# Optimization experiments

Measured on AMD Instinct MI355X. Metric: run time of the kernel, lower is better.

The kernel has to match this reference:

```python
import jax, jax.numpy as jnp
import numpy as np

N = 100000
E = 1600000
F_IN = 256
H1, C1 = 8, 8          # conv1: 8 heads x 8 channels -> 64
H2, C2 = 1, 32         # conv2: 1 head x num_classes
SLOPE = 0.2


def gat_conv(x, src, dst, n, W, a_src, a_dst, b, heads, out):
    # x: [n, f_in]; W: [f_in, heads*out]; a_src/a_dst: [heads, out]; b: [heads*out]
    h = (x @ W).reshape(n, heads, out)                       # [n, H, C]
    s = jnp.sum(h * a_src, axis=-1)                          # [n, H]
    d = jnp.sum(h * a_dst, axis=-1)                          # [n, H]
    e = jax.nn.leaky_relu(s[src] + d[dst], SLOPE)            # [e, H]
    m = jax.ops.segment_max(e, dst, num_segments=n)          # stable segment softmax
    ex = jnp.exp(e - m[dst])
    z = jax.ops.segment_sum(ex, dst, num_segments=n)
    alpha = ex / (z[dst] + 1e-16)                            # [e, H]
    msg = alpha[:, :, None] * h[src]                         # [e, H, C]
    agg = jax.ops.segment_sum(msg, dst, num_segments=n)      # [n, H, C]
    return agg.reshape(n, heads * out) + b


def setup_inputs() -> dict:
    key = jax.random.key(0)
    ks = jax.random.split(key, 10)
    x = jax.random.normal(ks[0], (N, F_IN), dtype=jnp.float32)
    edge_index = jax.random.randint(ks[1], (2, E), 0, N, dtype=jnp.int32)
    sc = 0.05
    W1 = jax.random.normal(ks[2], (F_IN, H1 * C1), dtype=jnp.float32) * sc
    att_src1 = jax.random.normal(ks[3], (H1, C1), dtype=jnp.float32) * sc
    att_dst1 = jax.random.normal(ks[4], (H1, C1), dtype=jnp.float32) * sc
    b1 = jnp.zeros((H1 * C1,), dtype=jnp.float32)
    W2 = jax.random.normal(ks[5], (H1 * C1, H2 * C2), dtype=jnp.float32) * sc
    att_src2 = jax.random.normal(ks[6], (H2, C2), dtype=jnp.float32) * sc
    att_dst2 = jax.random.normal(ks[7], (H2, C2), dtype=jnp.float32) * sc
    b2 = jnp.zeros((H2 * C2,), dtype=jnp.float32)
    return {"x": x, "edge_index": edge_index, "W1": W1, "att_src1": att_src1,
            "att_dst1": att_dst1, "b1": b1, "W2": W2, "att_src2": att_src2,
            "att_dst2": att_dst2, "b2": b2}


def reference(x, edge_index, W1, att_src1, att_dst1, b1, W2, att_src2, att_dst2, b2):
    # add self loops (PyG GATConv default)
    loops = jnp.arange(N, dtype=edge_index.dtype)
    src = jnp.concatenate([edge_index[0], loops])
    dst = jnp.concatenate([edge_index[1], loops])
    # dropout layers are identity in eval mode
    h = gat_conv(x, src, dst, N, W1, att_src1, att_dst1, b1, H1, C1)
    h = jax.nn.elu(h)
    h = gat_conv(h, src, dst, N, W2, att_src2, att_dst2, b2, H2, C2)
    return jax.nn.log_softmax(h, axis=1)
```

## Files before the change

### kernel.cpp

```cpp
#include <hip/hip_runtime.h>
#include <hip/hip_bf16.h>

#define N_NODES 100000
#define N_EDGES 1600000
#define N_TOT   (N_EDGES + N_NODES)
#define F_IN    256
#define F1      64
#define H1      8
#define C1      8
#define F2      32
#define SLOPE   0.2f
#define CHUNK   2048
#define NCH     ((N_NODES + CHUNK - 1) / CHUNK)

#define NB_G    ((N_NODES + 255) / 256)

#define EB      4096
#define NB1     ((N_EDGES + EB - 1) / EB)
#define BW      256
#define NBKT    ((N_NODES + BW - 1) / BW)

typedef unsigned int  uint;
typedef unsigned short ushort;
typedef __attribute__((ext_vector_type(8))) short bf16x8;
typedef __attribute__((ext_vector_type(4))) float f32x4;
typedef __attribute__((ext_vector_type(2))) float f32x2;

__device__ inline ushort f2bf(float f) {
    uint u = __float_as_uint(f);
    uint r = u + 0x7fffu + ((u >> 16) & 1u);
    return (ushort)(r >> 16);
}
__device__ inline float bflo(uint u) { return __uint_as_float(u << 16); }
__device__ inline float bfhi(uint u) { return __uint_as_float(u & 0xffff0000u); }
__device__ inline uint pk2bf(float a, float b) {
    __hip_bfloat162 h = __float22bfloat162_rn(make_float2(a, b));
    union { __hip_bfloat162 h; uint u; } cv; cv.h = h;
    return cv.u;
}

__device__ inline void bucket_bases(const int* __restrict__ colsum,
                                    int* sc, int* sb, int tid) {
    const int i0 = 2 * tid, i1 = 2 * tid + 1;
    const int a0 = (i0 < NBKT) ? colsum[i0] : 0;
    const int a1 = (i1 < NBKT) ? colsum[i1] : 0;
    sc[tid] = a0 + a1;
    __syncthreads();
    for (int off = 1; off < 256; off <<= 1) {
        int t = (tid >= off) ? sc[tid - off] : 0;
        __syncthreads();
        sc[tid] += t;
        __syncthreads();
    }
    const int excl = sc[tid] - (a0 + a1);
    if (i0 < NBKT)  sb[i0] = excl;
    if (i1 <= NBKT) sb[i1] = excl + a0;
    __syncthreads();
}

__global__ __launch_bounds__(256) void k_gemm1_p1(
        const float* __restrict__ x, const float* __restrict__ W1,
        const float* __restrict__ as1, const float* __restrict__ ad1,
        const int* __restrict__ ei,
        ushort* __restrict__ h1b, float* __restrict__ s1, float* __restrict__ d1,
        int* __restrict__ bcnt) {
    __shared__ union {
        ushort B[F_IN * F1];
        ushort S[4][64][66];
        int    H[NBKT];
    } sm;
    const int tid = threadIdx.x;

    if (blockIdx.x >= NB_G) {
        const int blk = blockIdx.x - NB_G;
        for (int j = tid; j < NBKT; j += 256) sm.H[j] = 0;
        __syncthreads();
        const int e0 = blk * EB;
        const int lim = (e0 + EB < N_EDGES) ? e0 + EB : N_EDGES;
        for (int i = e0 + tid; i < lim; i += 256)
            atomicAdd(&sm.H[ei[N_EDGES + i] >> 8], 1);
        __syncthreads();
        for (int j = tid; j < NBKT; j += 256)
            bcnt[j * NB1 + blk] = sm.H[j];
        return;
    }

    for (int i = 0; i < 64; ++i) {
        const int e = i * 256 + tid;
        const int k = e >> 6, n = e & 63;
        sm.B[((k >> 3) * 64 + n) * 8 + (k & 7)] = f2bf(W1[e]);
    }
    __syncthreads();

    const int wave = tid >> 6, lane = tid & 63;
    const int q = lane >> 4, ln = lane & 15;
    const int rowbase = blockIdx.x * 256 + wave * 64;

    f32x4 acc[4][4];
#pragma unroll
    for (int mt = 0; mt < 4; ++mt)
#pragma unroll
        for (int nt = 0; nt < 4; ++nt) acc[mt][nt] = (f32x4){0.f, 0.f, 0.f, 0.f};

    int rows[4];
#pragma unroll
    for (int mt = 0; mt < 4; ++mt) {
        const int r = rowbase + mt * 16 + ln;
        rows[mt] = r < N_NODES ? r : N_NODES - 1;
    }

    for (int t = 0; t < 8; ++t) {
        bf16x8 bfr[4];
#pragma unroll
        for (int nt = 0; nt < 4; ++nt)
            bfr[nt] = *(const bf16x8*)&sm.B[((t * 4 + q) * 64 + nt * 16 + ln) * 8];
#pragma unroll
        for (int mt = 0; mt < 4; ++mt) {
            const float4* ap = (const float4*)(x + (size_t)rows[mt] * F_IN + t * 32 + q * 8);
            const float4 a0 = ap[0], a1 = ap[1];
            uint4 au = make_uint4(pk2bf(a0.x, a0.y), pk2bf(a0.z, a0.w),
                                  pk2bf(a1.x, a1.y), pk2bf(a1.z, a1.w));
            bf16x8 af = *(bf16x8*)&au;
#pragma unroll
            for (int nt = 0; nt < 4; ++nt)
                acc[mt][nt] = __builtin_amdgcn_mfma_f32_16x16x32_bf16(
                                  af, bfr[nt], acc[mt][nt], 0, 0, 0);
        }
    }
    __syncthreads();

#pragma unroll
    for (int mt = 0; mt < 4; ++mt)
#pragma unroll
        for (int nt = 0; nt < 4; ++nt)
#pragma unroll
            for (int r = 0; r < 4; ++r)
                sm.S[wave][mt * 16 + q * 4 + r][nt * 16 + ln] = f2bf(acc[mt][nt][r]);
    __syncthreads();

    const int node = rowbase + lane;
    if (node >= N_NODES) return;
    const uint* srow = (const uint*)&sm.S[wave][lane][0];
    float sacc[H1], dacc[H1];
#pragma unroll
    for (int h = 0; h < H1; ++h) { sacc[h] = 0.f; dacc[h] = 0.f; }
    uint4* hout = (uint4*)(h1b + (size_t)node * F1);
#pragma unroll
    for (int p4 = 0; p4 < 8; ++p4) {
        const uint u0 = srow[p4 * 4 + 0], u1 = srow[p4 * 4 + 1];
        const uint u2 = srow[p4 * 4 + 2], u3 = srow[p4 * 4 + 3];
        hout[p4] = make_uint4(u0, u1, u2, u3);
        const float c[8] = {bflo(u0), bfhi(u0), bflo(u1), bfhi(u1),
                            bflo(u2), bfhi(u2), bflo(u3), bfhi(u3)};
#pragma unroll
        for (int j = 0; j < 8; ++j) {
            sacc[p4] += c[j] * as1[p4 * 8 + j];
            dacc[p4] += c[j] * ad1[p4 * 8 + j];
        }
    }
    float4* s4 = (float4*)(s1 + (size_t)node * H1);
    float4* d4 = (float4*)(d1 + (size_t)node * H1);
    s4[0] = make_float4(sacc[0], sacc[1], sacc[2], sacc[3]);
    s4[1] = make_float4(sacc[4], sacc[5], sacc[6], sacc[7]);
    d4[0] = make_float4(dacc[0], dacc[1], dacc[2], dacc[3]);
    d4[1] = make_float4(dacc[4], dacc[5], dacc[6], dacc[7]);
}

__global__ __launch_bounds__(64) void k_p2(
        int* __restrict__ bcnt, int* __restrict__ colsum) {
    const int col = blockIdx.x, lane = threadIdx.x;
    int carry = 0;
    for (int c0 = 0; c0 < NB1; c0 += 64) {
        const int idx = c0 + lane;
        const int v = (idx < NB1) ? bcnt[col * NB1 + idx] : 0;
        int s = v;
#pragma unroll
        for (int off = 1; off < 64; off <<= 1) {
            int u = __shfl_up(s, off);
            if (lane >= off) s += u;
        }
        if (idx < NB1) bcnt[col * NB1 + idx] = carry + s - v;
        carry += __shfl(s, 63);
    }
    if (lane == 0) colsum[col] = carry;
}

__global__ __launch_bounds__(256) void k_p3(
        const int* __restrict__ ei, const int* __restrict__ bcnt,
        const int* __restrict__ colsum, int2* __restrict__ tmp) {
    __shared__ int sc[256];
    __shared__ int cur[NBKT + 1];
    const int tid = threadIdx.x, blk = blockIdx.x;
    bucket_bases(colsum, sc, cur, tid);
    for (int b = tid; b < NBKT; b += 256) cur[b] += bcnt[b * NB1 + blk];
    __syncthreads();
    const int e0 = blk * EB;
    const int lim = (e0 + EB < N_EDGES) ? e0 + EB : N_EDGES;
    for (int i = e0 + tid; i < lim; i += 256) {
        const int s = ei[i], d = ei[N_EDGES + i];
        const int pos = atomicAdd(&cur[d >> 8], 1);
        tmp[pos] = make_int2(s, d);
    }
}

__global__ __launch_bounds__(256) void k_p4(
        const int2* __restrict__ tmp, const int* __restrict__ colsum,
        int* __restrict__ cnt) {
    __shared__ int sc[256];
    __shared__ int sb[NBKT + 1];
    __shared__ int h[BW];
    const int tid = threadIdx.x, b = blockIdx.x;
    bucket_bases(colsum, sc, sb, tid);
    h[tid] = 0;
    __syncthreads();
    const int lo = sb[b], hi = sb[b + 1];
    for (int i = lo + tid; i < hi; i += 256)
        atomicAdd(&h[tmp[i].y & (BW - 1)], 1);
    __syncthreads();
    const int n = b * BW + tid;
    if (n < N_NODES) cnt[n] = h[tid];
}

__global__ __launch_bounds__(256) void k_scan_a(
        const int* __restrict__ cnt, int* __restrict__ row_ptr,
        int* __restrict__ bsum) {
    __shared__ int sdata[256];
    const int tid = threadIdx.x;
    const int base = blockIdx.x * CHUNK + tid * 8;
    int v[8];
    int tot = 0;
#pragma unroll
    for (int j = 0; j < 8; ++j) {
        v[j] = (base + j < N_NODES) ? cnt[base + j] + 1 : 0;
        tot += v[j];
    }
    sdata[tid] = tot;
    __syncthreads();
    for (int off = 1; off < 256; off <<= 1) {
        int t = (tid >= off) ? sdata[tid - off] : 0;
        __syncthreads();
        sdata[tid] += t;
        __syncthreads();
    }
    int run = sdata[tid] - tot;
#pragma unroll
    for (int j = 0; j < 8; ++j) {
        if (base + j < N_NODES) row_ptr[base + j] = run;
        run += v[j];
    }
    if (tid == 255) bsum[blockIdx.x] = sdata[255];
}

__global__ __launch_bounds__(256) void k_scan_c2(
        int* __restrict__ row_ptr, const int* __restrict__ bsum,
        int* __restrict__ srcs) {
    __shared__ int pb[64];
    const int t = threadIdx.x;
    if (t < 64) {
        int v = (t < NCH) ? bsum[t] : 0;
        const int orig = v;
        for (int off = 1; off < 64; off <<= 1) {
            int u = __shfl_up(v, off);
            if (t >= off) v += u;
        }
        pb[t] = v - orig;
    }
    __syncthreads();
    const int i = blockIdx.x * 256 + t;
    if (i < N_NODES) {
        const int rp = row_ptr[i] + pb[i / CHUNK];
        row_ptr[i] = rp;
        srcs[rp] = i;
    } else if (i == N_NODES) row_ptr[N_NODES] = N_TOT;
}

__global__ __launch_bounds__(256) void k_p6(
        const int2* __restrict__ tmp, const int* __restrict__ colsum,
        const int* __restrict__ row_ptr, int* __restrict__ srcs) {
    __shared__ int sc[256];
    __shared__ int sb[NBKT + 1];
    __shared__ int rp[BW];
    __shared__ int cur[BW];
    const int tid = threadIdx.x, b = blockIdx.x;
    bucket_bases(colsum, sc, sb, tid);
    const int n = b * BW + tid;
    rp[tid] = (n < N_NODES) ? row_ptr[n] : 0;
    cur[tid] = 0;
    __syncthreads();
    const int lo = sb[b], hi = sb[b + 1];
    for (int i = lo + tid; i < hi; i += 256) {
        const int2 e = tmp[i];
        const int loc = e.y & (BW - 1);
        const int r = atomicAdd(&cur[loc], 1);
        srcs[rp[loc] + 1 + r] = e.x;
    }
}

__global__ __launch_bounds__(256) void k_agg1(
        const int* __restrict__ row_ptr, const int* __restrict__ srcs,
        const ushort* __restrict__ h1b, const float* __restrict__ s1,
        const float* __restrict__ d1, const float* __restrict__ b1,
        const float* __restrict__ W2, const float* __restrict__ as2,
        const float* __restrict__ ad2,
        ushort* __restrict__ h2b, float* __restrict__ s2,
        float* __restrict__ d2) {
    __shared__ float sx[4][64];
    const int wid = (blockIdx.x * 256 + threadIdx.x) >> 6;
    if (wid >= N_NODES) return;
    const int w = threadIdx.x >> 6;
    const int lane = threadIdx.x & 63;
    const int q = lane >> 3;
    const int c = lane & 7;
    const float dh = d1[(size_t)wid * H1 + c];
    const int beg = row_ptr[wid], end = row_ptr[wid + 1];
    const uint4* hv = (const uint4*)h1b;
    f32x2 A0 = {0.f, 0.f}, A1 = {0.f, 0.f}, A2 = {0.f, 0.f}, A3 = {0.f, 0.f};
    float z = 0.f;
    int i = beg + q;
    for (; i + 8 < end; i += 16) {
        const int sA = srcs[i], sB = srcs[i + 8];
        float eA = s1[(size_t)sA * H1 + c] + dh;
        float eB = s1[(size_t)sB * H1 + c] + dh;
        eA = fmaxf(eA, SLOPE * eA);
        eB = fmaxf(eB, SLOPE * eB);
        const float xA = __expf(eA), xB = __expf(eB);
        const uint4 UA = hv[(size_t)sA * 8 + c];
        const uint4 UB = hv[(size_t)sB * 8 + c];
        z += xA + xB;
        const f32x2 xa = {xA, xA}, xb = {xB, xB};
        A0 += xa * (f32x2){bflo(UA.x), bfhi(UA.x)};
        A1 += xa * (f32x2){bflo(UA.y), bfhi(UA.y)};
        A2 += xa * (f32x2){bflo(UA.z), bfhi(UA.z)};
        A3 += xa * (f32x2){bflo(UA.w), bfhi(UA.w)};
        A0 += xb * (f32x2){bflo(UB.x), bfhi(UB.x)};
        A1 += xb * (f32x2){bflo(UB.y), bfhi(UB.y)};
        A2 += xb * (f32x2){bflo(UB.z), bfhi(UB.z)};
        A3 += xb * (f32x2){bflo(UB.w), bfhi(UB.w)};
    }
    for (; i < end; i += 8) {
        const int sA = srcs[i];
        float eA = s1[(size_t)sA * H1 + c] + dh;
        eA = fmaxf(eA, SLOPE * eA);
        const float xA = __expf(eA);
        const uint4 UA = hv[(size_t)sA * 8 + c];
        z += xA;
        const f32x2 xa = {xA, xA};
        A0 += xa * (f32x2){bflo(UA.x), bfhi(UA.x)};
        A1 += xa * (f32x2){bflo(UA.y), bfhi(UA.y)};
        A2 += xa * (f32x2){bflo(UA.z), bfhi(UA.z)};
        A3 += xa * (f32x2){bflo(UA.w), bfhi(UA.w)};
    }
    f32x2 r0, r1;
    {
        const bool hi = lane & 8;
        f32x2 snd0 = hi ? A0 : A2, snd1 = hi ? A1 : A3;
        const f32x2 kp0 = hi ? A2 : A0, kp1 = hi ? A3 : A1;
        snd0.x = __shfl_xor(snd0.x, 8); snd0.y = __shfl_xor(snd0.y, 8);
        snd1.x = __shfl_xor(snd1.x, 8); snd1.y = __shfl_xor(snd1.y, 8);
        r0 = kp0 + snd0; r1 = kp1 + snd1;
    }
    {
        const bool hi = lane & 16;
        f32x2 snd = hi ? r0 : r1;
        const f32x2 kp = hi ? r1 : r0;
        snd.x = __shfl_xor(snd.x, 16); snd.y = __shfl_xor(snd.y, 16);
        r0 = kp + snd;
    }
    float sv;
    {
        const bool hi = lane & 32;
        float snd = hi ? r0.x : r0.y;
        const float kp = hi ? r0.y : r0.x;
        snd = __shfl_xor(snd, 32);
        sv = kp + snd;
    }
    z += __shfl_xor(z, 8); z += __shfl_xor(z, 16); z += __shfl_xor(z, 32);

    const int j = (((lane >> 3) & 1) << 2) | (((lane >> 4) & 1) << 1)
                | ((lane >> 5) & 1);
    const int xi = c * 8 + j;
    const float zi = 1.f / (z + 1e-16f);
    float xv = sv * zi + b1[xi];
    xv = xv > 0.f ? xv : __expf(xv) - 1.f;
    sx[w][xi] = xv;
    __builtin_amdgcn_wave_barrier();

    const int kh = lane >> 5;
    const int oc = lane & 31;
    const float4* sxv = (const float4*)&sx[w][kh * 32];
    const float* wp0 = W2 + (size_t)(kh * 32) * F2 + oc;
    float acc = 0.f;
#pragma unroll
    for (int k4 = 0; k4 < 8; ++k4) {
        const float4 xv4 = sxv[k4];
        const float* wp = wp0 + (size_t)k4 * 4 * F2;
        acc += xv4.x * wp[0]      + xv4.y * wp[F2]
             + xv4.z * wp[2 * F2] + xv4.w * wp[3 * F2];
    }
    acc += __shfl_xor(acc, 32);

    float sA2 = acc * as2[oc], dA2 = acc * ad2[oc];
#pragma unroll
    for (int off = 1; off <= 16; off <<= 1) {
        sA2 += __shfl_xor(sA2, off);
        dA2 += __shfl_xor(dA2, off);
    }
    const float accp = __shfl_xor(acc, 1);
    if (lane < 32 && !(lane & 1))
        *(uint*)&h2b[(size_t)wid * F2 + oc] = pk2bf(acc, accp);
    if (lane == 0) { s2[wid] = sA2; d2[wid] = dA2; }
}

__global__ __launch_bounds__(256) void k_agg2(
        const int* __restrict__ row_ptr, const int* __restrict__ srcs,
        const ushort* __restrict__ h2b, const float* __restrict__ s2,
        const float* __restrict__ d2, const float* __restrict__ b2,
        float* __restrict__ out) {
    const int wid = (blockIdx.x * 256 + threadIdx.x) >> 6;
    if (wid >= N_NODES) return;
    const int lane = threadIdx.x & 63;
    const int q = lane >> 2;
    const int c = lane & 3;
    const float dn = d2[wid];
    const int beg = row_ptr[wid], end = row_ptr[wid + 1];
    const uint4* hv = (const uint4*)h2b;
    f32x2 A0 = {0.f, 0.f}, A1 = {0.f, 0.f}, A2 = {0.f, 0.f}, A3 = {0.f, 0.f};
    float z = 0.f;
    int i = beg + q;
    for (; i + 16 < end; i += 32) {
        const int sA = srcs[i], sB = srcs[i + 16];
        float eA = s2[sA] + dn;
        float eB = s2[sB] + dn;
        eA = fmaxf(eA, SLOPE * eA);
        eB = fmaxf(eB, SLOPE * eB);
        const float xA = __expf(eA), xB = __expf(eB);
        const uint4 UA = hv[(size_t)sA * 4 + c];
        const uint4 UB = hv[(size_t)sB * 4 + c];
        z += xA + xB;
        const f32x2 xa = {xA, xA}, xb = {xB, xB};
        A0 += xa * (f32x2){bflo(UA.x), bfhi(UA.x)};
        A1 += xa * (f32x2){bflo(UA.y), bfhi(UA.y)};
        A2 += xa * (f32x2){bflo(UA.z), bfhi(UA.z)};
        A3 += xa * (f32x2){bflo(UA.w), bfhi(UA.w)};
        A0 += xb * (f32x2){bflo(UB.x), bfhi(UB.x)};
        A1 += xb * (f32x2){bflo(UB.y), bfhi(UB.y)};
        A2 += xb * (f32x2){bflo(UB.z), bfhi(UB.z)};
        A3 += xb * (f32x2){bflo(UB.w), bfhi(UB.w)};
    }
    for (; i < end; i += 16) {
        const int sA = srcs[i];
        float eA = s2[sA] + dn;
        eA = fmaxf(eA, SLOPE * eA);
        const float xA = __expf(eA);
        const uint4 UA = hv[(size_t)sA * 4 + c];
        z += xA;
        const f32x2 xa = {xA, xA};
        A0 += xa * (f32x2){bflo(UA.x), bfhi(UA.x)};
        A1 += xa * (f32x2){bflo(UA.y), bfhi(UA.y)};
        A2 += xa * (f32x2){bflo(UA.z), bfhi(UA.z)};
        A3 += xa * (f32x2){bflo(UA.w), bfhi(UA.w)};
    }
    f32x2 r0, r1;
    {
        const bool hi = lane & 4;
        f32x2 snd0 = hi ? A0 : A2, snd1 = hi ? A1 : A3;
        const f32x2 kp0 = hi ? A2 : A0, kp1 = hi ? A3 : A1;
        snd0.x = __shfl_xor(snd0.x, 4); snd0.y = __shfl_xor(snd0.y, 4);
        snd1.x = __shfl_xor(snd1.x, 4); snd1.y = __shfl_xor(snd1.y, 4);
        r0 = kp0 + snd0; r1 = kp1 + snd1;
    }
    {
        const bool hi = lane & 8;
        f32x2 snd = hi ? r0 : r1;
        const f32x2 kp = hi ? r1 : r0;
        snd.x = __shfl_xor(snd.x, 8); snd.y = __shfl_xor(snd.y, 8);
        r0 = kp + snd;
    }
    float sv;
    {
        const bool hi = lane & 16;
        float snd = hi ? r0.x : r0.y;
        const float kp = hi ? r0.y : r0.x;
        snd = __shfl_xor(snd, 16);
        sv = kp + snd;
    }
    sv += __shfl_xor(sv, 32);
    z += __shfl_xor(z, 4); z += __shfl_xor(z, 8);
    z += __shfl_xor(z, 16); z += __shfl_xor(z, 32);

    const int j = (((lane >> 2) & 1) << 2) | (((lane >> 3) & 1) << 1)
                | ((lane >> 4) & 1);
    const int elem = c * 8 + j;
    const float zi = 1.f / (z + 1e-16f);
    const float v = sv * zi + b2[elem];
    float m = v;
#pragma unroll
    for (int off = 1; off <= 16; off <<= 1) m = fmaxf(m, __shfl_xor(m, off));
    float ssum = __expf(v - m);
#pragma unroll
    for (int off = 1; off <= 16; off <<= 1) ssum += __shfl_xor(ssum, off);
    const float lse = m + __logf(ssum);
    if (lane < 32) out[(size_t)wid * F2 + elem] = v - lse;
}

extern "C" void kernel_launch(void* const* d_in, const int* in_sizes, int n_in,
                              void* d_out, int out_size, void* d_ws, size_t ws_size,
                              hipStream_t stream) {
    const float* x   = (const float*)d_in[0];
    const int*   ei  = (const int*)d_in[1];
    const float* W1  = (const float*)d_in[2];
    const float* as1 = (const float*)d_in[3];
    const float* ad1 = (const float*)d_in[4];
    const float* b1  = (const float*)d_in[5];
    const float* W2  = (const float*)d_in[6];
    const float* as2 = (const float*)d_in[7];
    const float* ad2 = (const float*)d_in[8];
    const float* b2  = (const float*)d_in[9];
    float* out = (float*)d_out;

    ushort* h1b = (ushort*)d_ws;
    ushort* h2b = h1b + (size_t)N_NODES * F1;
    float*  s1  = (float*)(h2b + (size_t)N_NODES * F2);
    float*  d1  = s1 + (size_t)N_NODES * H1;
    float*  s2  = d1 + (size_t)N_NODES * H1;
    float*  d2  = s2 + N_NODES;
    int2*   tmp = (int2*)(d2 + N_NODES);
    int* cnt     = (int*)(tmp + N_EDGES);
    int* row_ptr = cnt + N_NODES;
    int* bsum    = row_ptr + N_NODES + 1;
    int* colsum  = bsum + 64;
    int* bcnt    = colsum + NBKT;
    int* srcs    = bcnt + (size_t)NBKT * NB1;

    const int nb_w = (N_NODES * 64 + 255) / 256;

    k_gemm1_p1<<<NB_G + NB1, 256, 0, stream>>>(x, W1, as1, ad1, ei,
                                               h1b, s1, d1, bcnt);
    k_p2<<<NBKT, 64, 0, stream>>>(bcnt, colsum);
    k_p3<<<NB1, 256, 0, stream>>>(ei, bcnt, colsum, tmp);
    k_p4<<<NBKT, 256, 0, stream>>>(tmp, colsum, cnt);
    k_scan_a<<<NCH, 256, 0, stream>>>(cnt, row_ptr, bsum);
    k_scan_c2<<<(N_NODES + 256) / 256, 256, 0, stream>>>(row_ptr, bsum, srcs);
    k_p6<<<NBKT, 256, 0, stream>>>(tmp, colsum, row_ptr, srcs);
    k_agg1<<<nb_w, 256, 0, stream>>>(row_ptr, srcs, h1b, s1, d1, b1,
                                     W2, as2, ad2, h2b, s2, d2);
    k_agg2<<<nb_w, 256, 0, stream>>>(row_ptr, srcs, h2b, s2, d2, b2, out);
}
```

Measured before the change: 351.3 us.

## Fuse CSR build kernels, pack edge temp, and interleave s1 with h1 rows

Folds the per-bucket count, the two global scan kernels and the scatter into a single per-bucket kernel. Row offsets come from bucket bases plus a local scan, which removes three launches and a global cnt/row_ptr round trip. The temporary edge array is packed into one 32-bit word per edge (8-bit local dst, 24-bit src), halving that traffic. The layer-1 source logits s1 are stored in the same 160-byte row as the bf16 h1 features, so each gathered neighbour in aggregation touches one row instead of two separate arrays. The packing relies on node ids fitting in 24 bits and bucket width 256.

```diff
diff --git a/kernel.cpp b/kernel.cpp
--- a/kernel.cpp
+++ b/kernel.cpp
@@ -10,8 +10,6 @@
 #define C1      8
 #define F2      32
 #define SLOPE   0.2f
-#define CHUNK   2048
-#define NCH     ((N_NODES + CHUNK - 1) / CHUNK)
 
 #define NB_G    ((N_NODES + 255) / 256)
 
@@ -62,7 +60,7 @@
         const float* __restrict__ x, const float* __restrict__ W1,
         const float* __restrict__ as1, const float* __restrict__ ad1,
         const int* __restrict__ ei,
-        ushort* __restrict__ h1b, float* __restrict__ s1, float* __restrict__ d1,
+        uint* __restrict__ sh1, float* __restrict__ d1,
         int* __restrict__ bcnt) {
     __shared__ union {
         ushort B[F_IN * F1];
@@ -144,12 +142,12 @@
     float sacc[H1], dacc[H1];
 #pragma unroll
     for (int h = 0; h < H1; ++h) { sacc[h] = 0.f; dacc[h] = 0.f; }
-    uint4* hout = (uint4*)(h1b + (size_t)node * F1);
+    uint* rowp = sh1 + (size_t)node * 40;
 #pragma unroll
     for (int p4 = 0; p4 < 8; ++p4) {
         const uint u0 = srow[p4 * 4 + 0], u1 = srow[p4 * 4 + 1];
         const uint u2 = srow[p4 * 4 + 2], u3 = srow[p4 * 4 + 3];
-        hout[p4] = make_uint4(u0, u1, u2, u3);
+        ((uint4*)rowp)[2 + p4] = make_uint4(u0, u1, u2, u3);
         const float c[8] = {bflo(u0), bfhi(u0), bflo(u1), bfhi(u1),
                             bflo(u2), bfhi(u2), bflo(u3), bfhi(u3)};
 #pragma unroll
@@ -158,10 +156,9 @@
             dacc[p4] += c[j] * ad1[p4 * 8 + j];
         }
     }
-    float4* s4 = (float4*)(s1 + (size_t)node * H1);
+    ((float4*)rowp)[0] = make_float4(sacc[0], sacc[1], sacc[2], sacc[3]);
+    ((float4*)rowp)[1] = make_float4(sacc[4], sacc[5], sacc[6], sacc[7]);
     float4* d4 = (float4*)(d1 + (size_t)node * H1);
-    s4[0] = make_float4(sacc[0], sacc[1], sacc[2], sacc[3]);
-    s4[1] = make_float4(sacc[4], sacc[5], sacc[6], sacc[7]);
     d4[0] = make_float4(dacc[0], dacc[1], dacc[2], dacc[3]);
     d4[1] = make_float4(dacc[4], dacc[5], dacc[6], dacc[7]);
 }
@@ -187,7 +184,7 @@
 
 __global__ __launch_bounds__(256) void k_p3(
         const int* __restrict__ ei, const int* __restrict__ bcnt,
-        const int* __restrict__ colsum, int2* __restrict__ tmp) {
+        const int* __restrict__ colsum, uint* __restrict__ tmp) {
     __shared__ int sc[256];
     __shared__ int cur[NBKT + 1];
     const int tid = threadIdx.x, blk = blockIdx.x;
@@ -199,107 +196,54 @@
     for (int i = e0 + tid; i < lim; i += 256) {
         const int s = ei[i], d = ei[N_EDGES + i];
         const int pos = atomicAdd(&cur[d >> 8], 1);
-        tmp[pos] = make_int2(s, d);
-    }
-}
-
-__global__ __launch_bounds__(256) void k_p4(
-        const int2* __restrict__ tmp, const int* __restrict__ colsum,
-        int* __restrict__ cnt) {
+        tmp[pos] = ((uint)(d & 255) << 24) | (uint)s;
+    }
+}
+
+__global__ __launch_bounds__(256) void k_final(
+        const uint* __restrict__ tmp, const int* __restrict__ colsum,
+        int* __restrict__ row_ptr, int* __restrict__ srcs) {
     __shared__ int sc[256];
     __shared__ int sb[NBKT + 1];
-    __shared__ int h[BW];
-    const int tid = threadIdx.x, b = blockIdx.x;
-    bucket_bases(colsum, sc, sb, tid);
-    h[tid] = 0;
-    __syncthreads();
-    const int lo = sb[b], hi = sb[b + 1];
-    for (int i = lo + tid; i < hi; i += 256)
-        atomicAdd(&h[tmp[i].y & (BW - 1)], 1);
-    __syncthreads();
-    const int n = b * BW + tid;
-    if (n < N_NODES) cnt[n] = h[tid];
-}
-
-__global__ __launch_bounds__(256) void k_scan_a(
-        const int* __restrict__ cnt, int* __restrict__ row_ptr,
-        int* __restrict__ bsum) {
-    __shared__ int sdata[256];
-    const int tid = threadIdx.x;
-    const int base = blockIdx.x * CHUNK + tid * 8;
-    int v[8];
-    int tot = 0;
-#pragma unroll
-    for (int j = 0; j < 8; ++j) {
-        v[j] = (base + j < N_NODES) ? cnt[base + j] + 1 : 0;
-        tot += v[j];
-    }
-    sdata[tid] = tot;
-    __syncthreads();
-    for (int off = 1; off < 256; off <<= 1) {
-        int t = (tid >= off) ? sdata[tid - off] : 0;
-        __syncthreads();
-        sdata[tid] += t;
-        __syncthreads();
-    }
-    int run = sdata[tid] - tot;
-#pragma unroll
-    for (int j = 0; j < 8; ++j) {
-        if (base + j < N_NODES) row_ptr[base + j] = run;
-        run += v[j];
-    }
-    if (tid == 255) bsum[blockIdx.x] = sdata[255];
-}
-
-__global__ __launch_bounds__(256) void k_scan_c2(
-        int* __restrict__ row_ptr, const int* __restrict__ bsum,
-        int* __restrict__ srcs) {
-    __shared__ int pb[64];
-    const int t = threadIdx.x;
-    if (t < 64) {
-        int v = (t < NCH) ? bsum[t] : 0;
-        const int orig = v;
-        for (int off = 1; off < 64; off <<= 1) {
-            int u = __shfl_up(v, off);
-            if (t >= off) v += u;
-        }
-        pb[t] = v - orig;
-    }
-    __syncthreads();
-    const int i = blockIdx.x * 256 + t;
-    if (i < N_NODES) {
-        const int rp = row_ptr[i] + pb[i / CHUNK];
-        row_ptr[i] = rp;
-        srcs[rp] = i;
-    } else if (i == N_NODES) row_ptr[N_NODES] = N_TOT;
-}
-
-__global__ __launch_bounds__(256) void k_p6(
-        const int2* __restrict__ tmp, const int* __restrict__ colsum,
-        const int* __restrict__ row_ptr, int* __restrict__ srcs) {
-    __shared__ int sc[256];
-    __shared__ int sb[NBKT + 1];
-    __shared__ int rp[BW];
     __shared__ int cur[BW];
     const int tid = threadIdx.x, b = blockIdx.x;
     bucket_bases(colsum, sc, sb, tid);
+    cur[tid] = 0;
+    __syncthreads();
+    const int lo = sb[b], hi = sb[b + 1];
+    for (int i = lo + tid; i < hi; i += 256)
+        atomicAdd(&cur[tmp[i] >> 24], 1);
+    __syncthreads();
     const int n = b * BW + tid;
-    rp[tid] = (n < N_NODES) ? row_ptr[n] : 0;
-    cur[tid] = 0;
-    __syncthreads();
-    const int lo = sb[b], hi = sb[b + 1];
+    const int myc = cur[tid];
+    const int v = (n < N_NODES) ? myc + 1 : 0;
+    sc[tid] = v;
+    __syncthreads();
+    for (int off = 1; off < 256; off <<= 1) {
+        int t = (tid >= off) ? sc[tid - off] : 0;
+        __syncthreads();
+        sc[tid] += t;
+        __syncthreads();
+    }
+    const int rp = sb[b] + b * BW + (sc[tid] - v);
+    if (n < N_NODES) {
+        row_ptr[n] = rp;
+        srcs[rp] = n;
+    }
+    if (b == NBKT - 1 && tid == 255) row_ptr[N_NODES] = N_TOT;
+    cur[tid] = rp + 1;
+    __syncthreads();
     for (int i = lo + tid; i < hi; i += 256) {
-        const int2 e = tmp[i];
-        const int loc = e.y & (BW - 1);
-        const int r = atomicAdd(&cur[loc], 1);
-        srcs[rp[loc] + 1 + r] = e.x;
+        const uint u = tmp[i];
+        const int pos = atomicAdd(&cur[u >> 24], 1);
+        srcs[pos] = (int)(u & 0xFFFFFFu);
     }
 }
 
 __global__ __launch_bounds__(256) void k_agg1(
         const int* __restrict__ row_ptr, const int* __restrict__ srcs,
-        const ushort* __restrict__ h1b, const float* __restrict__ s1,
-        const float* __restrict__ d1, const float* __restrict__ b1,
+        const uint* __restrict__ sh1, const float* __restrict__ d1,
+        const float* __restrict__ b1,
         const float* __restrict__ W2, const float* __restrict__ as2,
         const float* __restrict__ ad2,
         ushort* __restrict__ h2b, float* __restrict__ s2,
@@ -311,21 +255,25 @@
     const int lane = threadIdx.x & 63;
     const int q = lane >> 3;
     const int c = lane & 7;
+    const int so = 4 * c;
+    const int ho = 32 + 16 * c;
     const float dh = d1[(size_t)wid * H1 + c];
     const int beg = row_ptr[wid], end = row_ptr[wid + 1];
-    const uint4* hv = (const uint4*)h1b;
+    const char* base = (const char*)sh1;
     f32x2 A0 = {0.f, 0.f}, A1 = {0.f, 0.f}, A2 = {0.f, 0.f}, A3 = {0.f, 0.f};
     float z = 0.f;
     int i = beg + q;
     for (; i + 8 < end; i += 16) {
         const int sA = srcs[i], sB = srcs[i + 8];
-        float eA = s1[(size_t)sA * H1 + c] + dh;
-        float eB = s1[(size_t)sB * H1 + c] + dh;
+        const char* rA = base + (size_t)sA * 160;
+        const char* rB = base + (size_t)sB * 160;
+        float eA = *(const float*)(rA + so) + dh;
+        float eB = *(const float*)(rB + so) + dh;
         eA = fmaxf(eA, SLOPE * eA);
         eB = fmaxf(eB, SLOPE * eB);
         const float xA = __expf(eA), xB = __expf(eB);
-        const uint4 UA = hv[(size_t)sA * 8 + c];
-        const uint4 UB = hv[(size_t)sB * 8 + c];
+        const uint4 UA = *(const uint4*)(rA + ho);
+        const uint4 UB = *(const uint4*)(rB + ho);
         z += xA + xB;
         const f32x2 xa = {xA, xA}, xb = {xB, xB};
         A0 += xa * (f32x2){bflo(UA.x), bfhi(UA.x)};
@@ -339,10 +287,11 @@
     }
     for (; i < end; i += 8) {
         const int sA = srcs[i];
-        float eA = s1[(size_t)sA * H1 + c] + dh;
+        const char* rA = base + (size_t)sA * 160;
+        float eA = *(const float*)(rA + so) + dh;
         eA = fmaxf(eA, SLOPE * eA);
         const float xA = __expf(eA);
-        const uint4 UA = hv[(size_t)sA * 8 + c];
+        const uint4 UA = *(const uint4*)(rA + ho);
         z += xA;
         const f32x2 xa = {xA, xA};
         A0 += xa * (f32x2){bflo(UA.x), bfhi(UA.x)};
@@ -518,31 +467,25 @@
     const float* b2  = (const float*)d_in[9];
     float* out = (float*)d_out;
 
-    ushort* h1b = (ushort*)d_ws;
-    ushort* h2b = h1b + (size_t)N_NODES * F1;
-    float*  s1  = (float*)(h2b + (size_t)N_NODES * F2);
-    float*  d1  = s1 + (size_t)N_NODES * H1;
+    uint*   sh1 = (uint*)d_ws;
+    ushort* h2b = (ushort*)(sh1 + (size_t)N_NODES * 40);
+    float*  d1  = (float*)(h2b + (size_t)N_NODES * F2);
     float*  s2  = d1 + (size_t)N_NODES * H1;
     float*  d2  = s2 + N_NODES;
-    int2*   tmp = (int2*)(d2 + N_NODES);
-    int* cnt     = (int*)(tmp + N_EDGES);
-    int* row_ptr = cnt + N_NODES;
-    int* bsum    = row_ptr + N_NODES + 1;
-    int* colsum  = bsum + 64;
+    uint*   tmp = (uint*)(d2 + N_NODES);
+    int* row_ptr = (int*)(tmp + N_EDGES);
+    int* colsum  = row_ptr + N_NODES + 1;
     int* bcnt    = colsum + NBKT;
     int* srcs    = bcnt + (size_t)NBKT * NB1;
 
     const int nb_w = (N_NODES * 64 + 255) / 256;
 
     k_gemm1_p1<<<NB_G + NB1, 256, 0, stream>>>(x, W1, as1, ad1, ei,
-                                               h1b, s1, d1, bcnt);
+                                               sh1, d1, bcnt);
     k_p2<<<NBKT, 64, 0, stream>>>(bcnt, colsum);
     k_p3<<<NB1, 256, 0, stream>>>(ei, bcnt, colsum, tmp);
-    k_p4<<<NBKT, 256, 0, stream>>>(tmp, colsum, cnt);
-    k_scan_a<<<NCH, 256, 0, stream>>>(cnt, row_ptr, bsum);
-    k_scan_c2<<<(N_NODES + 256) / 256, 256, 0, stream>>>(row_ptr, bsum, srcs);
-    k_p6<<<NBKT, 256, 0, stream>>>(tmp, colsum, row_ptr, srcs);
-    k_agg1<<<nb_w, 256, 0, stream>>>(row_ptr, srcs, h1b, s1, d1, b1,
+    k_final<<<NBKT, 256, 0, stream>>>(tmp, colsum, row_ptr, srcs);
+    k_agg1<<<nb_w, 256, 0, stream>>>(row_ptr, srcs, sh1, d1, b1,
                                      W2, as2, ad2, h2b, s2, d2);
     k_agg2<<<nb_w, 256, 0, stream>>>(row_ptr, srcs, h2b, s2, d2, b2, out);
 }
```

After: 342.2 us. -2.6%, faster.
